# Performance work log

Measured on AMD Instinct MI355X. Metric: run time of the kernel, lower is better.

Reference implementation:

```python
import jax, jax.numpy as jnp
import numpy as np

N_NODES = 100000
N_EDGES = 600000
N_GRAPHS = 64
BN_EPS = 1e-5


def setup_inputs() -> dict:
    key = jax.random.key(0)
    ks = jax.random.split(key, 32)
    inp = {
        "x": jax.random.normal(ks[0], (N_NODES, 128), dtype=jnp.float32),
        "edge_index": jax.random.randint(ks[1], (2, N_EDGES), 0, N_NODES, dtype=jnp.int64),
        "batch": jnp.sort(jax.random.randint(ks[2], (N_NODES,), 0, N_GRAPHS, dtype=jnp.int64)),
    }
    dims = [(128, 64, 64), (64, 64, 64), (64, 64, 96)]  # (in, hid, out) per GIN layer
    ki = 3
    for i, (d_in, d_hid, d_out) in enumerate(dims):
        inp[f"l{i}_w1"] = jax.random.normal(ks[ki], (d_in, d_hid), dtype=jnp.float32) * 0.05; ki += 1
        inp[f"l{i}_b1"] = jnp.zeros((d_hid,), dtype=jnp.float32)
        inp[f"l{i}_w2"] = jax.random.normal(ks[ki], (d_hid, d_out), dtype=jnp.float32) * 0.05; ki += 1
        inp[f"l{i}_b2"] = jnp.zeros((d_out,), dtype=jnp.float32)
        inp[f"bn{i}_g"] = jax.random.uniform(ks[ki], (d_out,), minval=0.5, maxval=1.5, dtype=jnp.float32); ki += 1
        inp[f"bn{i}_b"] = jax.random.normal(ks[ki], (d_out,), dtype=jnp.float32) * 0.05; ki += 1
        inp[f"bn{i}_m"] = jax.random.normal(ks[ki], (d_out,), dtype=jnp.float32) * 0.05; ki += 1
        inp[f"bn{i}_v"] = jax.random.uniform(ks[ki], (d_out,), minval=0.5, maxval=1.5, dtype=jnp.float32); ki += 1
    return inp


def _gin_layer(x, src, dst, w1, b1, w2, b2, g, bb, m, v):
    # GINConv (eps=0): h_i = MLP(x_i + sum_{j: j->i} x_j)
    aggr = jax.ops.segment_sum(x[src], dst, num_segments=N_NODES)
    h = x + aggr
    h = jax.nn.relu(h @ w1 + b1) @ w2 + b2
    # eval-mode BatchNorm1d + ReLU
    h = (h - m) * jax.lax.rsqrt(v + BN_EPS) * g + bb
    return jax.nn.relu(h)


def reference(x, edge_index, batch,
              l0_w1, l0_b1, l0_w2, l0_b2, bn0_g, bn0_b, bn0_m, bn0_v,
              l1_w1, l1_b1, l1_w2, l1_b2, bn1_g, bn1_b, bn1_m, bn1_v,
              l2_w1, l2_b1, l2_w2, l2_b2, bn2_g, bn2_b, bn2_m, bn2_v):
    src, dst = edge_index[0], edge_index[1]
    h = _gin_layer(x, src, dst, l0_w1, l0_b1, l0_w2, l0_b2, bn0_g, bn0_b, bn0_m, bn0_v)
    h = _gin_layer(h, src, dst, l1_w1, l1_b1, l1_w2, l1_b2, bn1_g, bn1_b, bn1_m, bn1_v)
    h = _gin_layer(h, src, dst, l2_w1, l2_b1, l2_w2, l2_b2, bn2_g, bn2_b, bn2_m, bn2_v)
    # global mean pool over graphs
    sums = jax.ops.segment_sum(h, batch, num_segments=N_GRAPHS)
    counts = jax.ops.segment_sum(jnp.ones((h.shape[0],), dtype=h.dtype), batch, num_segments=N_GRAPHS)
    return sums / jnp.maximum(counts, 1.0)[:, None]
```

## Files before the change

kernel.cpp:

```cpp
#include <hip/hip_runtime.h>

#define N_NODES 100000
#define N_GRAPHS 64
#define N_EDGES 600000
#define BN_EPS 1e-5f

typedef unsigned short bf16_t;

__device__ __forceinline__ unsigned short f2bf(float f) {
    unsigned int u = __float_as_uint(f);
    u += 0x7FFF + ((u >> 16) & 1);
    return (unsigned short)(u >> 16);
}
__device__ __forceinline__ uint2 pack4(float a, float b, float c, float d) {
    uint2 p;
    p.x = (unsigned)f2bf(a) | ((unsigned)f2bf(b) << 16);
    p.y = (unsigned)f2bf(c) | ((unsigned)f2bf(d) << 16);
    return p;
}
__device__ __forceinline__ void bf8_acc(uint4 q, float* acc) {
    acc[0] += __uint_as_float(q.x << 16);
    acc[1] += __uint_as_float(q.x & 0xFFFF0000u);
    acc[2] += __uint_as_float(q.y << 16);
    acc[3] += __uint_as_float(q.y & 0xFFFF0000u);
    acc[4] += __uint_as_float(q.z << 16);
    acc[5] += __uint_as_float(q.z & 0xFFFF0000u);
    acc[6] += __uint_as_float(q.w << 16);
    acc[7] += __uint_as_float(q.w & 0xFFFF0000u);
}

template <int SS>
__device__ __forceinline__ void gather_tile_to_lds512(
    const bf16_t* __restrict__ y, const int* __restrict__ rowptr,
    const int* __restrict__ eids, const float* __restrict__ b1,
    float* sT, long base, int n_nodes, int tid) {
    const uint4* yv = (const uint4*)y;
    const int f = tid & 7;
    const int lr = tid >> 3;
    float4 b0 = ((const float4*)b1)[f * 2];
    float4 b1v = ((const float4*)b1)[f * 2 + 1];
    long node = base + lr;
    float* sp = &sT[lr * SS + f * 8];
    if (node < n_nodes) {
        float acc[8] = {};
        bf8_acc(yv[node * 8 + f], acc);
        int bgn = rowptr[node], end = rowptr[node + 1];
        int i = bgn;
        for (; i + 3 < end; i += 4) {
            int s0 = eids[i], s1 = eids[i + 1], s2 = eids[i + 2], s3 = eids[i + 3];
            uint4 q0 = yv[(long)s0 * 8 + f];
            uint4 q1 = yv[(long)s1 * 8 + f];
            uint4 q2 = yv[(long)s2 * 8 + f];
            uint4 q3 = yv[(long)s3 * 8 + f];
            bf8_acc(q0, acc); bf8_acc(q1, acc); bf8_acc(q2, acc); bf8_acc(q3, acc);
        }
        for (; i < end; ++i) bf8_acc(yv[(long)eids[i] * 8 + f], acc);
        float4 o0, o1;
        o0.x = fmaxf(acc[0] + b0.x, 0.0f);
        o0.y = fmaxf(acc[1] + b0.y, 0.0f);
        o0.z = fmaxf(acc[2] + b0.z, 0.0f);
        o0.w = fmaxf(acc[3] + b0.w, 0.0f);
        o1.x = fmaxf(acc[4] + b1v.x, 0.0f);
        o1.y = fmaxf(acc[5] + b1v.y, 0.0f);
        o1.z = fmaxf(acc[6] + b1v.z, 0.0f);
        o1.w = fmaxf(acc[7] + b1v.w, 0.0f);
        *(float4*)sp = o0;
        *(float4*)(sp + 4) = o1;
    } else {
        float4 z = {0.0f, 0.0f, 0.0f, 0.0f};
        *(float4*)sp = z;
        *(float4*)(sp + 4) = z;
    }
}

__global__ void deg_hist_kernel(const int* __restrict__ dst,
                                int* __restrict__ deg, int n_edges) {
    int e = blockIdx.x * blockDim.x + threadIdx.x;
    if (e < n_edges) atomicAdd(&deg[dst[e]], 1);
}

__global__ __launch_bounds__(1024)
void scan_fused_kernel(const int* __restrict__ deg, int* __restrict__ rowptr,
                       int* __restrict__ agg, int n, int total) {
    __shared__ int s[1024];
    __shared__ int s2[128];
    __shared__ int offset_sh;
    const int b = blockIdx.x;
    const int i = b * 1024 + threadIdx.x;
    int v = (i < n) ? deg[i] : 0;
    s[threadIdx.x] = v;
    __syncthreads();
    for (int off = 1; off < 1024; off <<= 1) {
        int t = (threadIdx.x >= (unsigned)off) ? s[threadIdx.x - off] : 0;
        __syncthreads();
        s[threadIdx.x] += t;
        __syncthreads();
    }
    if (threadIdx.x == 1023) atomicExch(&agg[b], s[1023]);
    if (threadIdx.x < b) {
        int val;
        do { val = atomicAdd(&agg[threadIdx.x], 0); } while (val == -1);
        s2[threadIdx.x] = val;
    }
    __syncthreads();
    if (threadIdx.x == 0) {
        int off = 0;
        for (int k = 0; k < b; ++k) off += s2[k];
        offset_sh = off;
    }
    __syncthreads();
    const int off = offset_sh;
    if (i < n) rowptr[i] = off + s[threadIdx.x] - v;
    else if (i == n) rowptr[n] = total;
}

__global__ __launch_bounds__(256)
void fill_pre_kernel(const int* __restrict__ src, const int* __restrict__ dst,
                     const int* __restrict__ rowptr, int* __restrict__ cursor,
                     int* __restrict__ eids, const int* __restrict__ batch,
                     int* __restrict__ gstart,
                     const float* __restrict__ x, const float* __restrict__ w1T,
                     bf16_t* __restrict__ y, int n_edges, int n_nodes) {
    __shared__ float w1s[64 * 128];
    const int bq = blockIdx.x / 5, br = blockIdx.x % 5;

    if (br < 3) {
        int e = (bq * 3 + br) * 256 + threadIdx.x;
        if (e < n_edges) {
            int t = dst[e];
            int pos = rowptr[t] + atomicAdd(&cursor[t], 1);
            eids[pos] = src[e];
        }
        if (e < n_nodes) {
            if (e == 0) {
                for (int g = 0; g <= batch[0]; ++g) gstart[g] = 0;
            } else {
                int b0 = batch[e - 1], b1 = batch[e];
                for (int g = b0 + 1; g <= b1; ++g) gstart[g] = e;
            }
            if (e == n_nodes - 1) {
                for (int g = batch[e] + 1; g <= N_GRAPHS; ++g) gstart[g] = n_nodes;
            }
        }
        return;
    }

    const int gb = bq * 2 + (br - 3);
    const long base = (long)gb * 64;
    if (base >= n_nodes) return;
    const int tid = threadIdx.x;

    const float4* gw1 = (const float4*)w1T;
    for (int i4 = tid; i4 < 16 * 128; i4 += 256) {
        int row = i4 >> 5, k4 = i4 & 31;
        *(float4*)&w1s[row * 128 + ((k4 ^ ((row >> 2) & 7)) << 2)] = gw1[i4];
    }
    __syncthreads();

    const int jg = tid & 15, ng = tid >> 4, xw = jg & 7;
    const float* wp = &w1s[(jg * 4) * 128];
    const float4* xv = (const float4*)x;
    long r[4];
    #pragma unroll
    for (int i = 0; i < 4; ++i) {
        long rr = base + ng * 4 + i;
        r[i] = (rr < n_nodes) ? rr : (n_nodes - 1);
    }
    float acc[4][4] = {};
    #pragma unroll 4
    for (int k4 = 0; k4 < 32; ++k4) {
        const int ko = (k4 ^ xw) << 2;
        float4 w0 = *(const float4*)&wp[0 * 128 + ko];
        float4 w1v = *(const float4*)&wp[1 * 128 + ko];
        float4 w2v = *(const float4*)&wp[2 * 128 + ko];
        float4 w3v = *(const float4*)&wp[3 * 128 + ko];
        #pragma unroll
        for (int i = 0; i < 4; ++i) {
            float4 a = xv[r[i] * 32 + k4];
            acc[i][0] = fmaf(a.x, w0.x, fmaf(a.y, w0.y, fmaf(a.z, w0.z, fmaf(a.w, w0.w, acc[i][0]))));
            acc[i][1] = fmaf(a.x, w1v.x, fmaf(a.y, w1v.y, fmaf(a.z, w1v.z, fmaf(a.w, w1v.w, acc[i][1]))));
            acc[i][2] = fmaf(a.x, w2v.x, fmaf(a.y, w2v.y, fmaf(a.z, w2v.z, fmaf(a.w, w2v.w, acc[i][2]))));
            acc[i][3] = fmaf(a.x, w3v.x, fmaf(a.y, w3v.y, fmaf(a.z, w3v.z, fmaf(a.w, w3v.w, acc[i][3]))));
        }
    }
    #pragma unroll
    for (int i = 0; i < 4; ++i) {
        long n = base + ng * 4 + i;
        if (n < n_nodes) {
            *(uint2*)(y + n * 64 + jg * 4) = pack4(acc[i][0], acc[i][1], acc[i][2], acc[i][3]);
        }
    }
}

struct LayerPrep {
    const float *w1, *w2, *b2, *g, *bb, *m, *v;
    float *w1T, *w2sT, *bias2;
    int DIN, DOUT;
};
struct PrepAll { LayerPrep l[3]; };

__global__ void prep_all_kernel(PrepAll pa, int* __restrict__ deg,
                                int* __restrict__ cursor, float* __restrict__ out_zero,
                                int* __restrict__ agg) {
    LayerPrep P = pa.l[blockIdx.y];
    int i = blockIdx.x * blockDim.x + threadIdx.x;
    if (blockIdx.y == 0) {
        int stride = gridDim.x * blockDim.x;
        for (int k = i; k < N_NODES; k += stride) { deg[k] = 0; cursor[k] = 0; }
        for (int k = i; k < N_GRAPHS * 96; k += stride) out_zero[k] = 0.0f;
        if (i < 128) agg[i] = -1;
    }
    if (i < 64 * P.DIN) {
        int j = i / P.DIN, k = i % P.DIN;
        P.w1T[i] = P.w1[k * 64 + j];
    }
    int i2 = i - 64 * P.DIN;
    if (i2 >= 0 && i2 < P.DOUT * 64) {
        int c = i2 / 64, j = i2 % 64;
        float s = P.g[c] * rsqrtf(P.v[c] + BN_EPS);
        P.w2sT[i2] = P.w2[j * P.DOUT + c] * s;
    }
    int i3 = i2 - P.DOUT * 64;
    if (i3 >= 0 && i3 < P.DOUT) {
        float s = P.g[i3] * rsqrtf(P.v[i3] + BN_EPS);
        P.bias2[i3] = (P.b2[i3] - P.m[i3]) * s + P.bb[i3];
    }
}

__global__ __launch_bounds__(512)
void fused_gather_mid_kernel(const bf16_t* __restrict__ y,
                             const int* __restrict__ rowptr,
                             const int* __restrict__ eids,
                             const float* __restrict__ b1,
                             const float* __restrict__ w2sT,
                             const float* __restrict__ bias2,
                             const float* __restrict__ w1nT,
                             bf16_t* __restrict__ ynext, int n_nodes) {
    constexpr int SS = 68;
    __shared__ float sT[64 * SS];
    __shared__ float wbuf[64 * 64];
    const int tid = threadIdx.x;
    const long base = (long)blockIdx.x * 64;

    const float4* gw2 = (const float4*)w2sT;
    for (int i4 = tid; i4 < 16 * 64; i4 += 512) {
        int row = i4 >> 4, k4 = i4 & 15;
        *(float4*)&wbuf[row * 64 + ((k4 ^ ((row >> 2) & 7)) << 2)] = gw2[i4];
    }
    gather_tile_to_lds512<SS>(y, rowptr, eids, b1, sT, base, n_nodes, tid);
    __syncthreads();

    const int jg = tid & 15, ng = tid >> 4, xw = jg & 7;

    float h[2][4];
    {
        const float* wp = &wbuf[(jg * 4) * 64];
        float acc[2][4] = {};
        #pragma unroll 4
        for (int k4 = 0; k4 < 16; ++k4) {
            const int ko = (k4 ^ xw) << 2;
            float4 w0 = *(const float4*)&wp[0 * 64 + ko];
            float4 w1v = *(const float4*)&wp[1 * 64 + ko];
            float4 w2v = *(const float4*)&wp[2 * 64 + ko];
            float4 w3v = *(const float4*)&wp[3 * 64 + ko];
            #pragma unroll
            for (int i = 0; i < 2; ++i) {
                float4 a = *(const float4*)&sT[(ng * 2 + i) * SS + k4 * 4];
                acc[i][0] = fmaf(a.x, w0.x, fmaf(a.y, w0.y, fmaf(a.z, w0.z, fmaf(a.w, w0.w, acc[i][0]))));
                acc[i][1] = fmaf(a.x, w1v.x, fmaf(a.y, w1v.y, fmaf(a.z, w1v.z, fmaf(a.w, w1v.w, acc[i][1]))));
                acc[i][2] = fmaf(a.x, w2v.x, fmaf(a.y, w2v.y, fmaf(a.z, w2v.z, fmaf(a.w, w2v.w, acc[i][2]))));
                acc[i][3] = fmaf(a.x, w3v.x, fmaf(a.y, w3v.y, fmaf(a.z, w3v.z, fmaf(a.w, w3v.w, acc[i][3]))));
            }
        }
        float4 bv = *(const float4*)&bias2[jg * 4];
        #pragma unroll
        for (int i = 0; i < 2; ++i) {
            h[i][0] = fmaxf(acc[i][0] + bv.x, 0.0f);
            h[i][1] = fmaxf(acc[i][1] + bv.y, 0.0f);
            h[i][2] = fmaxf(acc[i][2] + bv.z, 0.0f);
            h[i][3] = fmaxf(acc[i][3] + bv.w, 0.0f);
        }
    }
    __syncthreads();

    #pragma unroll
    for (int i = 0; i < 2; ++i) {
        float4 hv = {h[i][0], h[i][1], h[i][2], h[i][3]};
        *(float4*)&sT[(ng * 2 + i) * SS + jg * 4] = hv;
    }
    const float4* gw1n = (const float4*)w1nT;
    for (int i4 = tid; i4 < 16 * 64; i4 += 512) {
        int row = i4 >> 4, k4 = i4 & 15;
        *(float4*)&wbuf[row * 64 + ((k4 ^ ((row >> 2) & 7)) << 2)] = gw1n[i4];
    }
    __syncthreads();

    {
        const float* ap = &sT[(ng * 2) * SS];
        const float* wp = &wbuf[(jg * 4) * 64];
        float acc[2][4] = {};
        #pragma unroll 4
        for (int k4 = 0; k4 < 16; ++k4) {
            const int ko = (k4 ^ xw) << 2;
            float4 w0 = *(const float4*)&wp[0 * 64 + ko];
            float4 w1v = *(const float4*)&wp[1 * 64 + ko];
            float4 w2v = *(const float4*)&wp[2 * 64 + ko];
            float4 w3v = *(const float4*)&wp[3 * 64 + ko];
            #pragma unroll
            for (int i = 0; i < 2; ++i) {
                float4 a = *(const float4*)&ap[i * SS + k4 * 4];
                acc[i][0] = fmaf(a.x, w0.x, fmaf(a.y, w0.y, fmaf(a.z, w0.z, fmaf(a.w, w0.w, acc[i][0]))));
                acc[i][1] = fmaf(a.x, w1v.x, fmaf(a.y, w1v.y, fmaf(a.z, w1v.z, fmaf(a.w, w1v.w, acc[i][1]))));
                acc[i][2] = fmaf(a.x, w2v.x, fmaf(a.y, w2v.y, fmaf(a.z, w2v.z, fmaf(a.w, w2v.w, acc[i][2]))));
                acc[i][3] = fmaf(a.x, w3v.x, fmaf(a.y, w3v.y, fmaf(a.z, w3v.z, fmaf(a.w, w3v.w, acc[i][3]))));
            }
        }
        #pragma unroll
        for (int i = 0; i < 2; ++i) {
            long n = base + ng * 2 + i;
            if (n < n_nodes) {
                *(uint2*)(ynext + n * 64 + jg * 4) = pack4(acc[i][0], acc[i][1], acc[i][2], acc[i][3]);
            }
        }
    }
}

__global__ __launch_bounds__(512)
void fused_gather_final_kernel(const bf16_t* __restrict__ y,
                               const int* __restrict__ rowptr,
                               const int* __restrict__ eids,
                               const float* __restrict__ b1,
                               const float* __restrict__ w2sT,
                               const float* __restrict__ bias2,
                               const int* __restrict__ batch,
                               const int* __restrict__ gstart,
                               float* __restrict__ out, int n_nodes) {
    constexpr int CPT = 6;
    constexpr int SS = 68;
    __shared__ float w2s[96 * 64];
    __shared__ float tbuf[64 * SS];
    const int tid = threadIdx.x;
    const long base = (long)blockIdx.x * 64;

    const float4* gw2 = (const float4*)w2sT;
    for (int i4 = tid; i4 < 96 * 16; i4 += 512) {
        int row = i4 >> 4, k4 = i4 & 15;
        *(float4*)&w2s[row * 64 + ((k4 ^ ((row / CPT) & 7)) << 2)] = gw2[i4];
    }
    gather_tile_to_lds512<SS>(y, rowptr, eids, b1, tbuf, base, n_nodes, tid);
    __syncthreads();

    const int cg_ = tid & 15, ng = tid >> 4, xw = cg_ & 7;
    const float* wp = &w2s[(cg_ * CPT) * 64];
    float acc[2][CPT] = {};
    #pragma unroll 4
    for (int k4 = 0; k4 < 16; ++k4) {
        const int ko = (k4 ^ xw) << 2;
        float4 wv[CPT];
        #pragma unroll
        for (int c = 0; c < CPT; ++c) wv[c] = *(const float4*)&wp[c * 64 + ko];
        #pragma unroll
        for (int i = 0; i < 2; ++i) {
            float4 h = *(const float4*)&tbuf[(ng * 2 + i) * SS + k4 * 4];
            #pragma unroll
            for (int c = 0; c < CPT; ++c)
                acc[i][c] = fmaf(h.x, wv[c].x, fmaf(h.y, wv[c].y, fmaf(h.z, wv[c].z, fmaf(h.w, wv[c].w, acc[i][c]))));
        }
    }
    float bv[CPT];
    #pragma unroll
    for (int c = 0; c < CPT; ++c) bv[c] = bias2[cg_ * CPT + c];
    __syncthreads();
    #pragma unroll
    for (int i = 0; i < 2; ++i) {
        long n = base + ng * 2 + i;
        float* hp = &w2s[(ng * 2 + i) * 96 + cg_ * CPT];
        if (n < n_nodes) {
            #pragma unroll
            for (int c = 0; c < CPT; ++c) hp[c] = fmaxf(acc[i][c] + bv[c], 0.0f);
        } else {
            #pragma unroll
            for (int c = 0; c < CPT; ++c) hp[c] = 0.0f;
        }
    }
    __syncthreads();

    if (tid < 96) {
        int limit = (int)((n_nodes - base < 64) ? (n_nodes - base) : 64);
        int gcur = batch[base];
        float s = 0.0f;
        for (int r = 0; r < limit; ++r) {
            int g = batch[base + r];
            if (g != gcur) {
                float inv = 1.0f / fmaxf((float)(gstart[gcur + 1] - gstart[gcur]), 1.0f);
                atomicAdd(&out[gcur * 96 + tid], s * inv);
                s = 0.0f;
                gcur = g;
            }
            s += w2s[r * 96 + tid];
        }
        float inv = 1.0f / fmaxf((float)(gstart[gcur + 1] - gstart[gcur]), 1.0f);
        atomicAdd(&out[gcur * 96 + tid], s * inv);
    }
}

static inline int cdiv_l(long a, int b) { return (int)((a + b - 1) / b); }

extern "C" void kernel_launch(void* const* d_in, const int* in_sizes, int n_in,
                              void* d_out, int out_size, void* d_ws, size_t ws_size,
                              hipStream_t stream) {
    const float* x     = (const float*)d_in[0];
    const int*   ei    = (const int*)d_in[1];
    const int*   src   = ei;
    const int*   dst   = ei + N_EDGES;
    const int*   batch = (const int*)d_in[2];

    const float* P[3][8];
    int p = 3;
    for (int l = 0; l < 3; ++l)
        for (int q = 0; q < 8; ++q)
            P[l][q] = (const float*)d_in[p++];

    const long NP = N_NODES + 128;
    char* wsb   = (char*)d_ws;
    bf16_t* yA  = (bf16_t*)wsb;
    bf16_t* yB  = yA + NP * 64;
    float* q    = (float*)(yB + NP * 64);
    float* w1T[3], *w2sT[3], *bias2[3];
    for (int l = 0; l < 3; ++l) {
        w1T[l] = q;   q += 64 * 128;
        w2sT[l] = q;  q += 96 * 64;
        bias2[l] = q; q += 96;
    }
    int* gstart   = (int*)q;
    int* deg      = gstart + 72;
    int* cursor   = deg + N_NODES;
    int* partials = cursor + N_NODES;
    int* rowptr   = partials + 128;
    int* eids     = rowptr + (N_NODES + 1);

    const int B = 256;
    const int DIN[3]  = {128, 64, 64};
    const int DOUT[3] = {64, 64, 96};

    PrepAll pa;
    for (int l = 0; l < 3; ++l) {
        pa.l[l].w1 = P[l][0]; pa.l[l].w2 = P[l][2]; pa.l[l].b2 = P[l][3];
        pa.l[l].g = P[l][4];  pa.l[l].bb = P[l][5]; pa.l[l].m = P[l][6];
        pa.l[l].v = P[l][7];
        pa.l[l].w1T = w1T[l]; pa.l[l].w2sT = w2sT[l]; pa.l[l].bias2 = bias2[l];
        pa.l[l].DIN = DIN[l]; pa.l[l].DOUT = DOUT[l];
    }
    dim3 pgrid(cdiv_l(64 * 128 + 96 * 64 + 96, B), 3);
    prep_all_kernel<<<pgrid, B, 0, stream>>>(pa, deg, cursor, (float*)d_out, partials);

    deg_hist_kernel<<<cdiv_l(N_EDGES, B), B, 0, stream>>>(dst, deg, N_EDGES);
    int nblk = cdiv_l(N_NODES + 1, 1024);
    scan_fused_kernel<<<nblk, 1024, 0, stream>>>(deg, rowptr, partials, N_NODES, N_EDGES);

    const int nfill  = cdiv_l(N_EDGES, B);
    const int ngemm  = cdiv_l(N_NODES, 64);
    const int ngrp_f = cdiv_l(nfill, 3);
    const int ngrp_g = cdiv_l(ngemm, 2);
    const int ngroups = (ngrp_f > ngrp_g) ? ngrp_f : ngrp_g;
    fill_pre_kernel<<<ngroups * 5, B, 0, stream>>>(
        src, dst, rowptr, cursor, eids, batch, gstart,
        x, w1T[0], yA, N_EDGES, N_NODES);

    const int ntiles = cdiv_l(N_NODES, 64);

    fused_gather_mid_kernel<<<ntiles, 512, 0, stream>>>(
        yA, rowptr, eids, P[0][1], w2sT[0], bias2[0], w1T[1], yB, N_NODES);
    fused_gather_mid_kernel<<<ntiles, 512, 0, stream>>>(
        yB, rowptr, eids, P[1][1], w2sT[1], bias2[1], w1T[2], yA, N_NODES);
    fused_gather_final_kernel<<<ntiles, 512, 0, stream>>>(
        yA, rowptr, eids, P[2][1], w2sT[2], bias2[2], batch, gstart,
        (float*)d_out, N_NODES);
}
```

Before: 357.3 us.

## Sort tile nodes by degree for gather balance and widen fill/pre-GEMM blocks

In the gather helper, each 64-node tile now computes node degrees into shared memory, ranks them, and assigns nodes to 8-thread groups in descending degree order. The aim is to cut divergence from mixed degrees within a wavefront. It adds two barriers and a 64-iteration rank loop per tile. Separately, the fused fill/pre-GEMM kernel moves to 512-thread blocks, with 3 fill blocks and 4 GEMM blocks per group of 7 and 2 rows per thread instead of 4. That lowers per-thread register use but reloads the shared weights from more blocks.

```diff
diff --git a/kernel.cpp b/kernel.cpp
--- a/kernel.cpp
+++ b/kernel.cpp
@@ -33,10 +33,27 @@
 __device__ __forceinline__ void gather_tile_to_lds512(
     const bf16_t* __restrict__ y, const int* __restrict__ rowptr,
     const int* __restrict__ eids, const float* __restrict__ b1,
-    float* sT, long base, int n_nodes, int tid) {
+    float* sT, int* degs, int* perm, long base, int n_nodes, int tid) {
+    if (tid < 64) {
+        long node = base + tid;
+        degs[tid] = (node < n_nodes) ? (rowptr[node + 1] - rowptr[node]) : -1;
+    }
+    __syncthreads();
+    if (tid < 64) {
+        int d = degs[tid];
+        int r = 0;
+        #pragma unroll 8
+        for (int j = 0; j < 64; ++j) {
+            int dj = degs[j];
+            r += (dj > d || (dj == d && j < tid)) ? 1 : 0;
+        }
+        perm[r] = tid;
+    }
+    __syncthreads();
+
     const uint4* yv = (const uint4*)y;
     const int f = tid & 7;
-    const int lr = tid >> 3;
+    const int lr = perm[tid >> 3];
     float4 b0 = ((const float4*)b1)[f * 2];
     float4 b1v = ((const float4*)b1)[f * 2 + 1];
     long node = base + lr;
@@ -114,7 +131,7 @@
     else if (i == n) rowptr[n] = total;
 }
 
-__global__ __launch_bounds__(256)
+__global__ __launch_bounds__(512)
 void fill_pre_kernel(const int* __restrict__ src, const int* __restrict__ dst,
                      const int* __restrict__ rowptr, int* __restrict__ cursor,
                      int* __restrict__ eids, const int* __restrict__ batch,
@@ -122,10 +139,11 @@
                      const float* __restrict__ x, const float* __restrict__ w1T,
                      bf16_t* __restrict__ y, int n_edges, int n_nodes) {
     __shared__ float w1s[64 * 128];
-    const int bq = blockIdx.x / 5, br = blockIdx.x % 5;
+    const int bq = blockIdx.x / 7, br = blockIdx.x % 7;
+    const int tid = threadIdx.x;
 
     if (br < 3) {
-        int e = (bq * 3 + br) * 256 + threadIdx.x;
+        int e = (bq * 3 + br) * 512 + tid;
         if (e < n_edges) {
             int t = dst[e];
             int pos = rowptr[t] + atomicAdd(&cursor[t], 1);
@@ -145,13 +163,12 @@
         return;
     }
 
-    const int gb = bq * 2 + (br - 3);
+    const int gb = bq * 4 + (br - 3);
     const long base = (long)gb * 64;
     if (base >= n_nodes) return;
-    const int tid = threadIdx.x;
 
     const float4* gw1 = (const float4*)w1T;
-    for (int i4 = tid; i4 < 16 * 128; i4 += 256) {
+    for (int i4 = tid; i4 < 16 * 128; i4 += 512) {
         int row = i4 >> 5, k4 = i4 & 31;
         *(float4*)&w1s[row * 128 + ((k4 ^ ((row >> 2) & 7)) << 2)] = gw1[i4];
     }
@@ -160,13 +177,13 @@
     const int jg = tid & 15, ng = tid >> 4, xw = jg & 7;
     const float* wp = &w1s[(jg * 4) * 128];
     const float4* xv = (const float4*)x;
-    long r[4];
+    long r[2];
     #pragma unroll
-    for (int i = 0; i < 4; ++i) {
-        long rr = base + ng * 4 + i;
+    for (int i = 0; i < 2; ++i) {
+        long rr = base + ng * 2 + i;
         r[i] = (rr < n_nodes) ? rr : (n_nodes - 1);
     }
-    float acc[4][4] = {};
+    float acc[2][4] = {};
     #pragma unroll 4
     for (int k4 = 0; k4 < 32; ++k4) {
         const int ko = (k4 ^ xw) << 2;
@@ -175,7 +192,7 @@
         float4 w2v = *(const float4*)&wp[2 * 128 + ko];
         float4 w3v = *(const float4*)&wp[3 * 128 + ko];
         #pragma unroll
-        for (int i = 0; i < 4; ++i) {
+        for (int i = 0; i < 2; ++i) {
             float4 a = xv[r[i] * 32 + k4];
             acc[i][0] = fmaf(a.x, w0.x, fmaf(a.y, w0.y, fmaf(a.z, w0.z, fmaf(a.w, w0.w, acc[i][0]))));
             acc[i][1] = fmaf(a.x, w1v.x, fmaf(a.y, w1v.y, fmaf(a.z, w1v.z, fmaf(a.w, w1v.w, acc[i][1]))));
@@ -184,8 +201,8 @@
         }
     }
     #pragma unroll
-    for (int i = 0; i < 4; ++i) {
-        long n = base + ng * 4 + i;
+    for (int i = 0; i < 2; ++i) {
+        long n = base + ng * 2 + i;
         if (n < n_nodes) {
             *(uint2*)(y + n * 64 + jg * 4) = pack4(acc[i][0], acc[i][1], acc[i][2], acc[i][3]);
         }
@@ -239,6 +256,8 @@
     constexpr int SS = 68;
     __shared__ float sT[64 * SS];
     __shared__ float wbuf[64 * 64];
+    __shared__ int degs[64];
+    __shared__ int perm[64];
     const int tid = threadIdx.x;
     const long base = (long)blockIdx.x * 64;
 
@@ -247,7 +266,7 @@
         int row = i4 >> 4, k4 = i4 & 15;
         *(float4*)&wbuf[row * 64 + ((k4 ^ ((row >> 2) & 7)) << 2)] = gw2[i4];
     }
-    gather_tile_to_lds512<SS>(y, rowptr, eids, b1, sT, base, n_nodes, tid);
+    gather_tile_to_lds512<SS>(y, rowptr, eids, b1, sT, degs, perm, base, n_nodes, tid);
     __syncthreads();
 
     const int jg = tid & 15, ng = tid >> 4, xw = jg & 7;
@@ -339,6 +358,8 @@
     constexpr int SS = 68;
     __shared__ float w2s[96 * 64];
     __shared__ float tbuf[64 * SS];
+    __shared__ int degs[64];
+    __shared__ int perm[64];
     const int tid = threadIdx.x;
     const long base = (long)blockIdx.x * 64;
 
@@ -347,7 +368,7 @@
         int row = i4 >> 4, k4 = i4 & 15;
         *(float4*)&w2s[row * 64 + ((k4 ^ ((row / CPT) & 7)) << 2)] = gw2[i4];
     }
-    gather_tile_to_lds512<SS>(y, rowptr, eids, b1, tbuf, base, n_nodes, tid);
+    gather_tile_to_lds512<SS>(y, rowptr, eids, b1, tbuf, degs, perm, base, n_nodes, tid);
     __syncthreads();
 
     const int cg_ = tid & 15, ng = tid >> 4, xw = cg_ & 7;
@@ -458,12 +479,12 @@
     int nblk = cdiv_l(N_NODES + 1, 1024);
     scan_fused_kernel<<<nblk, 1024, 0, stream>>>(deg, rowptr, partials, N_NODES, N_EDGES);
 
-    const int nfill  = cdiv_l(N_EDGES, B);
+    const int nfill  = cdiv_l(N_EDGES, 512);
     const int ngemm  = cdiv_l(N_NODES, 64);
     const int ngrp_f = cdiv_l(nfill, 3);
-    const int ngrp_g = cdiv_l(ngemm, 2);
+    const int ngrp_g = cdiv_l(ngemm, 4);
     const int ngroups = (ngrp_f > ngrp_g) ? ngrp_f : ngrp_g;
-    fill_pre_kernel<<<ngroups * 5, B, 0, stream>>>(
+    fill_pre_kernel<<<ngroups * 7, 512, 0, stream>>>(
         src, dst, rowptr, cursor, eids, batch, gstart,
         x, w1T[0], yA, N_EDGES, N_NODES);
 
```

Result: slower. 372.5 us (+4.3%).

## Remap dense MLP thread mapping to one node per lane with wave-uniform weights

Applied to the files above, without the earlier changes.

Changes the in-block dense matmul mapping in the mid and final fused kernels so each lane owns one node and each wavefront owns a contiguous slice of output columns. Weight reads from LDS then use the same address across the wave (a broadcast), so the XOR swizzle is dropped. The final kernel also rotates its staging layout so the pooling reads do not hit bank conflicts. The trade-off is more accumulators per thread (8 or 12), which adds register pressure, and activation rows are now read per lane with a 68-float stride.

```diff
diff --git a/kernel.cpp b/kernel.cpp
--- a/kernel.cpp
+++ b/kernel.cpp
@@ -242,85 +242,71 @@
     const int tid = threadIdx.x;
     const long base = (long)blockIdx.x * 64;
 
-    const float4* gw2 = (const float4*)w2sT;
-    for (int i4 = tid; i4 < 16 * 64; i4 += 512) {
-        int row = i4 >> 4, k4 = i4 & 15;
-        *(float4*)&wbuf[row * 64 + ((k4 ^ ((row >> 2) & 7)) << 2)] = gw2[i4];
+    {
+        const float4* gw2 = (const float4*)w2sT;
+        float4* wb4 = (float4*)wbuf;
+        for (int i4 = tid; i4 < 16 * 64; i4 += 512) wb4[i4] = gw2[i4];
     }
     gather_tile_to_lds512<SS>(y, rowptr, eids, b1, sT, base, n_nodes, tid);
     __syncthreads();
 
-    const int jg = tid & 15, ng = tid >> 4, xw = jg & 7;
-
-    float h[2][4];
-    {
-        const float* wp = &wbuf[(jg * 4) * 64];
-        float acc[2][4] = {};
+    const int W = tid >> 6, L = tid & 63;
+
+    float h[8];
+    {
+        float acc[8] = {};
+        const float* ap = &sT[L * SS];
+        const float* wp = &wbuf[(W * 8) * 64];
         #pragma unroll 4
         for (int k4 = 0; k4 < 16; ++k4) {
-            const int ko = (k4 ^ xw) << 2;
-            float4 w0 = *(const float4*)&wp[0 * 64 + ko];
-            float4 w1v = *(const float4*)&wp[1 * 64 + ko];
-            float4 w2v = *(const float4*)&wp[2 * 64 + ko];
-            float4 w3v = *(const float4*)&wp[3 * 64 + ko];
+            float4 a = *(const float4*)&ap[k4 * 4];
             #pragma unroll
-            for (int i = 0; i < 2; ++i) {
-                float4 a = *(const float4*)&sT[(ng * 2 + i) * SS + k4 * 4];
-                acc[i][0] = fmaf(a.x, w0.x, fmaf(a.y, w0.y, fmaf(a.z, w0.z, fmaf(a.w, w0.w, acc[i][0]))));
-                acc[i][1] = fmaf(a.x, w1v.x, fmaf(a.y, w1v.y, fmaf(a.z, w1v.z, fmaf(a.w, w1v.w, acc[i][1]))));
-                acc[i][2] = fmaf(a.x, w2v.x, fmaf(a.y, w2v.y, fmaf(a.z, w2v.z, fmaf(a.w, w2v.w, acc[i][2]))));
-                acc[i][3] = fmaf(a.x, w3v.x, fmaf(a.y, w3v.y, fmaf(a.z, w3v.z, fmaf(a.w, w3v.w, acc[i][3]))));
-            }
-        }
-        float4 bv = *(const float4*)&bias2[jg * 4];
-        #pragma unroll
-        for (int i = 0; i < 2; ++i) {
-            h[i][0] = fmaxf(acc[i][0] + bv.x, 0.0f);
-            h[i][1] = fmaxf(acc[i][1] + bv.y, 0.0f);
-            h[i][2] = fmaxf(acc[i][2] + bv.z, 0.0f);
-            h[i][3] = fmaxf(acc[i][3] + bv.w, 0.0f);
-        }
-    }
-    __syncthreads();
-
-    #pragma unroll
-    for (int i = 0; i < 2; ++i) {
-        float4 hv = {h[i][0], h[i][1], h[i][2], h[i][3]};
-        *(float4*)&sT[(ng * 2 + i) * SS + jg * 4] = hv;
-    }
-    const float4* gw1n = (const float4*)w1nT;
-    for (int i4 = tid; i4 < 16 * 64; i4 += 512) {
-        int row = i4 >> 4, k4 = i4 & 15;
-        *(float4*)&wbuf[row * 64 + ((k4 ^ ((row >> 2) & 7)) << 2)] = gw1n[i4];
-    }
-    __syncthreads();
-
-    {
-        const float* ap = &sT[(ng * 2) * SS];
-        const float* wp = &wbuf[(jg * 4) * 64];
-        float acc[2][4] = {};
+            for (int c = 0; c < 8; ++c) {
+                float4 wv = *(const float4*)&wp[c * 64 + k4 * 4];
+                acc[c] = fmaf(a.x, wv.x, fmaf(a.y, wv.y, fmaf(a.z, wv.z, fmaf(a.w, wv.w, acc[c]))));
+            }
+        }
+        float4 b0 = *(const float4*)&bias2[W * 8];
+        float4 b1v = *(const float4*)&bias2[W * 8 + 4];
+        h[0] = fmaxf(acc[0] + b0.x, 0.0f);
+        h[1] = fmaxf(acc[1] + b0.y, 0.0f);
+        h[2] = fmaxf(acc[2] + b0.z, 0.0f);
+        h[3] = fmaxf(acc[3] + b0.w, 0.0f);
+        h[4] = fmaxf(acc[4] + b1v.x, 0.0f);
+        h[5] = fmaxf(acc[5] + b1v.y, 0.0f);
+        h[6] = fmaxf(acc[6] + b1v.z, 0.0f);
+        h[7] = fmaxf(acc[7] + b1v.w, 0.0f);
+    }
+    __syncthreads();
+
+    {
+        float4 h0 = {h[0], h[1], h[2], h[3]};
+        float4 h1 = {h[4], h[5], h[6], h[7]};
+        *(float4*)&sT[L * SS + W * 8] = h0;
+        *(float4*)&sT[L * SS + W * 8 + 4] = h1;
+        const float4* gw1n = (const float4*)w1nT;
+        float4* wb4 = (float4*)wbuf;
+        for (int i4 = tid; i4 < 16 * 64; i4 += 512) wb4[i4] = gw1n[i4];
+    }
+    __syncthreads();
+
+    {
+        float acc[8] = {};
+        const float* ap = &sT[L * SS];
+        const float* wp = &wbuf[(W * 8) * 64];
         #pragma unroll 4
         for (int k4 = 0; k4 < 16; ++k4) {
-            const int ko = (k4 ^ xw) << 2;
-            float4 w0 = *(const float4*)&wp[0 * 64 + ko];
-            float4 w1v = *(const float4*)&wp[1 * 64 + ko];
-            float4 w2v = *(const float4*)&wp[2 * 64 + ko];
-            float4 w3v = *(const float4*)&wp[3 * 64 + ko];
+            float4 a = *(const float4*)&ap[k4 * 4];
             #pragma unroll
-            for (int i = 0; i < 2; ++i) {
-                float4 a = *(const float4*)&ap[i * SS + k4 * 4];
-                acc[i][0] = fmaf(a.x, w0.x, fmaf(a.y, w0.y, fmaf(a.z, w0.z, fmaf(a.w, w0.w, acc[i][0]))));
-                acc[i][1] = fmaf(a.x, w1v.x, fmaf(a.y, w1v.y, fmaf(a.z, w1v.z, fmaf(a.w, w1v.w, acc[i][1]))));
-                acc[i][2] = fmaf(a.x, w2v.x, fmaf(a.y, w2v.y, fmaf(a.z, w2v.z, fmaf(a.w, w2v.w, acc[i][2]))));
-                acc[i][3] = fmaf(a.x, w3v.x, fmaf(a.y, w3v.y, fmaf(a.z, w3v.z, fmaf(a.w, w3v.w, acc[i][3]))));
-            }
-        }
-        #pragma unroll
-        for (int i = 0; i < 2; ++i) {
-            long n = base + ng * 2 + i;
-            if (n < n_nodes) {
-                *(uint2*)(ynext + n * 64 + jg * 4) = pack4(acc[i][0], acc[i][1], acc[i][2], acc[i][3]);
-            }
+            for (int c = 0; c < 8; ++c) {
+                float4 wv = *(const float4*)&wp[c * 64 + k4 * 4];
+                acc[c] = fmaf(a.x, wv.x, fmaf(a.y, wv.y, fmaf(a.z, wv.z, fmaf(a.w, wv.w, acc[c]))));
+            }
+        }
+        long n = base + L;
+        if (n < n_nodes) {
+            *(uint2*)(ynext + n * 64 + W * 8) = pack4(acc[0], acc[1], acc[2], acc[3]);
+            *(uint2*)(ynext + n * 64 + W * 8 + 4) = pack4(acc[4], acc[5], acc[6], acc[7]);
         }
     }
 }
@@ -335,52 +321,47 @@
                                const int* __restrict__ batch,
                                const int* __restrict__ gstart,
                                float* __restrict__ out, int n_nodes) {
-    constexpr int CPT = 6;
     constexpr int SS = 68;
     __shared__ float w2s[96 * 64];
     __shared__ float tbuf[64 * SS];
     const int tid = threadIdx.x;
     const long base = (long)blockIdx.x * 64;
 
-    const float4* gw2 = (const float4*)w2sT;
-    for (int i4 = tid; i4 < 96 * 16; i4 += 512) {
-        int row = i4 >> 4, k4 = i4 & 15;
-        *(float4*)&w2s[row * 64 + ((k4 ^ ((row / CPT) & 7)) << 2)] = gw2[i4];
+    {
+        const float4* gw2 = (const float4*)w2sT;
+        float4* wb4 = (float4*)w2s;
+        for (int i4 = tid; i4 < 96 * 16; i4 += 512) wb4[i4] = gw2[i4];
     }
     gather_tile_to_lds512<SS>(y, rowptr, eids, b1, tbuf, base, n_nodes, tid);
     __syncthreads();
 
-    const int cg_ = tid & 15, ng = tid >> 4, xw = cg_ & 7;
-    const float* wp = &w2s[(cg_ * CPT) * 64];
-    float acc[2][CPT] = {};
-    #pragma unroll 4
-    for (int k4 = 0; k4 < 16; ++k4) {
-        const int ko = (k4 ^ xw) << 2;
-        float4 wv[CPT];
+    const int W = tid >> 6, L = tid & 63;
+
+    float acc[12] = {};
+    {
+        const float* ap = &tbuf[L * SS];
+        const float* wp = &w2s[(W * 12) * 64];
+        #pragma unroll 2
+        for (int k4 = 0; k4 < 16; ++k4) {
+            float4 a = *(const float4*)&ap[k4 * 4];
+            #pragma unroll
+            for (int c = 0; c < 12; ++c) {
+                float4 wv = *(const float4*)&wp[c * 64 + k4 * 4];
+                acc[c] = fmaf(a.x, wv.x, fmaf(a.y, wv.y, fmaf(a.z, wv.z, fmaf(a.w, wv.w, acc[c]))));
+            }
+        }
+    }
+    float bv[12];
+    #pragma unroll
+    for (int c = 0; c < 12; ++c) bv[c] = bias2[W * 12 + c];
+    __syncthreads();
+
+    {
+        long n = base + L;
         #pragma unroll
-        for (int c = 0; c < CPT; ++c) wv[c] = *(const float4*)&wp[c * 64 + ko];
-        #pragma unroll
-        for (int i = 0; i < 2; ++i) {
-            float4 h = *(const float4*)&tbuf[(ng * 2 + i) * SS + k4 * 4];
-            #pragma unroll
-            for (int c = 0; c < CPT; ++c)
-                acc[i][c] = fmaf(h.x, wv[c].x, fmaf(h.y, wv[c].y, fmaf(h.z, wv[c].z, fmaf(h.w, wv[c].w, acc[i][c]))));
-        }
-    }
-    float bv[CPT];
-    #pragma unroll
-    for (int c = 0; c < CPT; ++c) bv[c] = bias2[cg_ * CPT + c];
-    __syncthreads();
-    #pragma unroll
-    for (int i = 0; i < 2; ++i) {
-        long n = base + ng * 2 + i;
-        float* hp = &w2s[(ng * 2 + i) * 96 + cg_ * CPT];
-        if (n < n_nodes) {
-            #pragma unroll
-            for (int c = 0; c < CPT; ++c) hp[c] = fmaxf(acc[i][c] + bv[c], 0.0f);
-        } else {
-            #pragma unroll
-            for (int c = 0; c < CPT; ++c) hp[c] = 0.0f;
+        for (int c = 0; c < 12; ++c) {
+            float hv = (n < n_nodes) ? fmaxf(acc[c] + bv[c], 0.0f) : 0.0f;
+            w2s[L * 96 + ((W * 12 + c + L * 4) % 96)] = hv;
         }
     }
     __syncthreads();
@@ -397,7 +378,7 @@
                 s = 0.0f;
                 gcur = g;
             }
-            s += w2s[r * 96 + tid];
+            s += w2s[r * 96 + ((tid + r * 4) % 96)];
         }
         float inv = 1.0f / fmaxf((float)(gstart[gcur + 1] - gstart[gcur]), 1.0f);
         atomicAdd(&out[gcur * 96 + tid], s * inv);
```

Result: slower. 436.3 us (+22.1%).

## Partition CSR fill by destination range per XCD to localize atomics

Applied to the files above, without the earlier changes.

The edge-scatter phase of the fill kernel is restructured. Each block is tied to an XCD via blockIdx&7 and scans a 2048-edge chunk, but only inserts edges whose destination lies in that XCD's eighth of the node range. The goal is to keep atomics on cursor and the writes to eids within one XCD's L2 and avoid cross-die contention. The cost is that every edge is read eight times, once by each XCD group, which adds redundant dst loads and branch divergence.

```diff
diff --git a/kernel.cpp b/kernel.cpp
--- a/kernel.cpp
+++ b/kernel.cpp
@@ -4,6 +4,9 @@
 #define N_GRAPHS 64
 #define N_EDGES 600000
 #define BN_EPS 1e-5f
+
+#define FILL_NSUB 293
+#define FILL_PER  2048
 
 typedef unsigned short bf16_t;
 
@@ -125,21 +128,33 @@
     const int bq = blockIdx.x / 5, br = blockIdx.x % 5;
 
     if (br < 3) {
-        int e = (bq * 3 + br) * 256 + threadIdx.x;
-        if (e < n_edges) {
-            int t = dst[e];
-            int pos = rowptr[t] + atomicAdd(&cursor[t], 1);
-            eids[pos] = src[e];
-        }
-        if (e < n_nodes) {
-            if (e == 0) {
+        const int fb = bq * 3 + br;
+        int e0 = fb * 256 + threadIdx.x;
+        if (e0 < n_nodes) {
+            if (e0 == 0) {
                 for (int g = 0; g <= batch[0]; ++g) gstart[g] = 0;
             } else {
-                int b0 = batch[e - 1], b1 = batch[e];
-                for (int g = b0 + 1; g <= b1; ++g) gstart[g] = e;
-            }
-            if (e == n_nodes - 1) {
-                for (int g = batch[e] + 1; g <= N_GRAPHS; ++g) gstart[g] = n_nodes;
+                int b0 = batch[e0 - 1], b1 = batch[e0];
+                for (int g = b0 + 1; g <= b1; ++g) gstart[g] = e0;
+            }
+            if (e0 == n_nodes - 1) {
+                for (int g = batch[e0] + 1; g <= N_GRAPHS; ++g) gstart[g] = n_nodes;
+            }
+        }
+        const int xcd = fb & 7;
+        const int sub = fb >> 3;
+        if (sub < FILL_NSUB) {
+            const int lo = xcd * (N_NODES / 8);
+            const int hi = lo + (N_NODES / 8);
+            int beg = sub * FILL_PER;
+            int end = beg + FILL_PER;
+            if (end > n_edges) end = n_edges;
+            for (int e = beg + threadIdx.x; e < end; e += 256) {
+                int t = dst[e];
+                if (t >= lo && t < hi) {
+                    int pos = rowptr[t] + atomicAdd(&cursor[t], 1);
+                    eids[pos] = src[e];
+                }
             }
         }
         return;
```

Measured after the change: 353.9 us. About the same (-0.9%).
